# Kernel tuning notes

Measured on AMD Instinct MI355X. Metric: run time of the kernel, lower is better.

Reference implementation:

```python
import jax, jax.numpy as jnp
import numpy as np

DIM = 512
HEADS = 8
DIM_HEAD = 64
INNER = HEADS * DIM_HEAD  # 512
LN_EPS = 1e-5


def setup_inputs() -> dict:
    key = jax.random.key(0)
    ks = jax.random.split(key, 6)
    b, n = 2, 2048
    x = jax.random.normal(ks[0], (b, n, DIM), dtype=jnp.float32)
    # to_qkv: Linear(dim, inner*3, bias=False); torch weight is [out,in], apply as x @ W.T
    w_qkv = jax.random.normal(ks[1], (3 * INNER, DIM), dtype=jnp.float32) * (DIM ** -0.5)
    reattn_w = jax.random.normal(ks[2], (HEADS, HEADS), dtype=jnp.float32)
    ln_g = jnp.ones((HEADS,), dtype=jnp.float32)
    ln_b = jnp.zeros((HEADS,), dtype=jnp.float32)
    w_out = jax.random.normal(ks[3], (DIM, INNER), dtype=jnp.float32) * (INNER ** -0.5)
    b_out = jnp.zeros((DIM,), dtype=jnp.float32)
    return {"x": x, "w_qkv": w_qkv, "reattn_w": reattn_w,
            "ln_g": ln_g, "ln_b": ln_b, "w_out": w_out, "b_out": b_out}


def reference(x, w_qkv, reattn_w, ln_g, ln_b, w_out, b_out):
    b, n, _ = x.shape
    scale = DIM_HEAD ** -0.5
    qkv = x @ w_qkv.T  # [b, n, 3*inner]
    q, k, v = jnp.split(qkv, 3, axis=-1)
    # b n (h d) -> b h n d
    split_heads = lambda t: t.reshape(b, n, HEADS, DIM_HEAD).transpose(0, 2, 1, 3)
    q, k, v = split_heads(q), split_heads(k), split_heads(v)
    dots = jnp.einsum('bhid,bhjd->bhij', q, k) * scale
    attn = jax.nn.softmax(dots, axis=-1)
    # re-attention: cross-head mixing then LayerNorm over head dim
    attn = jnp.einsum('bhij,hg->bgij', attn, reattn_w)
    a = attn.transpose(0, 2, 3, 1)  # b i j h
    mu = jnp.mean(a, axis=-1, keepdims=True)
    var = jnp.mean((a - mu) ** 2, axis=-1, keepdims=True)
    a = (a - mu) * jax.lax.rsqrt(var + LN_EPS) * ln_g + ln_b
    attn = a.transpose(0, 3, 1, 2)  # b h i j
    out = jnp.einsum('bhij,bhjd->bhid', attn, v)
    out = out.transpose(0, 2, 1, 3).reshape(b, n, INNER)
    out = out @ w_out.T + b_out  # dropout p=0 -> identity
    return out
```

## Files before the change

kernel.cpp:

```cpp
#include <hip/hip_runtime.h>
#include <hip/hip_bf16.h>


typedef __attribute__((ext_vector_type(8))) short bfx8;
typedef __attribute__((ext_vector_type(4))) float f32x4;
typedef unsigned short u16;
typedef unsigned int u32;

#define QSCALE 0.18033688011112042f

static __device__ inline u16 f2bf(float f) {
  union { float f; unsigned u; } cv; cv.f = f;
  unsigned u = cv.u;
  u += 0x7fffu + ((u >> 16) & 1u);
  return (u16)(u >> 16);
}
static __device__ inline u32 cvtpk(float lo, float hi) {
  u32 d; asm("v_cvt_pk_bf16_f32 %0, %1, %2" : "=v"(d) : "v"(lo), "v"(hi)); return d;
}
static __device__ inline float fexp2(float x) {
  float r; asm("v_exp_f32 %0, %1" : "=v"(r) : "v"(x)); return r;
}
static __device__ inline float flog2(float x) {
  float r; asm("v_log_f32 %0, %1" : "=v"(r) : "v"(x)); return r;
}

__global__ __launch_bounds__(256) void convert3(
    const float* __restrict__ x, const float* __restrict__ wq,
    const float* __restrict__ wo,
    u16* __restrict__ xb, u16* __restrict__ wqb, u16* __restrict__ wob) {
  int e = (blockIdx.x * 256 + threadIdx.x) * 4;
  const float* src; u16* dst; int off;
  if (e < 2097152)      { src = x;  dst = xb;  off = e; }
  else if (e < 2883584) { src = wq; dst = wqb; off = e - 2097152; }
  else                  { src = wo; dst = wob; off = e - 2883584; }
  float4 v = *(const float4*)&src[off];
  ushort4 o; o.x = f2bf(v.x); o.y = f2bf(v.y); o.z = f2bf(v.z); o.w = f2bf(v.w);
  *(ushort4*)&dst[off] = o;
}

__global__ __launch_bounds__(256) void gemm_qkv(
    const u16* __restrict__ A, const u16* __restrict__ B,
    u16* __restrict__ qb, u16* __restrict__ kb, u16* __restrict__ vtb) {
  __shared__ u16 As[128 * 32];
  __shared__ u16 Bs[128 * 32];
  const int t = threadIdx.x, lane = t & 63;
  const int wm = (t >> 6) >> 1, wn = (t >> 6) & 1;
  const int m0 = blockIdx.y * 128, n0 = blockIdx.x * 128;
  const int li = lane & 15, lg = lane >> 4;
  const int rowA = t >> 2, kb8 = (t & 3) * 8;
  f32x4 acc[4][4] = {};
  for (int k0 = 0; k0 < 512; k0 += 32) {
    __syncthreads();
    *(bfx8*)&As[rowA * 32 + kb8]        = *(const bfx8*)&A[(size_t)(m0 + rowA) * 512 + k0 + kb8];
    *(bfx8*)&As[(rowA + 64) * 32 + kb8] = *(const bfx8*)&A[(size_t)(m0 + rowA + 64) * 512 + k0 + kb8];
    *(bfx8*)&Bs[rowA * 32 + kb8]        = *(const bfx8*)&B[(size_t)(n0 + rowA) * 512 + k0 + kb8];
    *(bfx8*)&Bs[(rowA + 64) * 32 + kb8] = *(const bfx8*)&B[(size_t)(n0 + rowA + 64) * 512 + k0 + kb8];
    __syncthreads();
    bfx8 af[4], bf_[4];
#pragma unroll
    for (int mi = 0; mi < 4; mi++)
      af[mi] = *(const bfx8*)&As[(wm * 64 + mi * 16 + li) * 32 + lg * 8];
#pragma unroll
    for (int ni = 0; ni < 4; ni++)
      bf_[ni] = *(const bfx8*)&Bs[(wn * 64 + ni * 16 + li) * 32 + lg * 8];
#pragma unroll
    for (int mi = 0; mi < 4; mi++)
#pragma unroll
      for (int ni = 0; ni < 4; ni++)
        acc[mi][ni] = __builtin_amdgcn_mfma_f32_16x16x32_bf16(af[mi], bf_[ni], acc[mi][ni], 0, 0, 0);
  }
#pragma unroll
  for (int mi = 0; mi < 4; mi++) {
#pragma unroll
    for (int ni = 0; ni < 4; ni++) {
      const int nc  = n0 + wn * 64 + ni * 16 + li;
      const int mrb = m0 + wm * 64 + mi * 16 + lg * 4;
      const int part = nc >> 9, within = nc & 511;
      const int h = within >> 6, d = within & 63;
      const int bb = mrb >> 11, ii = mrb & 2047;
      if (part == 0) {
#pragma unroll
        for (int r = 0; r < 4; r++)
          qb[(((size_t)bb * 8 + h) * 2048 + ii + r) * 64 + d] = f2bf(acc[mi][ni][r] * QSCALE);
      } else if (part == 1) {
#pragma unroll
        for (int r = 0; r < 4; r++)
          kb[(((size_t)bb * 8 + h) * 2048 + ii + r) * 64 + d] = f2bf(acc[mi][ni][r]);
      } else {
        ushort4 u;
        u.x = f2bf(acc[mi][ni][0]); u.y = f2bf(acc[mi][ni][1]);
        u.z = f2bf(acc[mi][ni][2]); u.w = f2bf(acc[mi][ni][3]);
        *(ushort4*)&vtb[(((size_t)bb * 8 + h) * 64 + d) * 2048 + ii] = u;
      }
    }
  }
}

__global__ __launch_bounds__(256) void passA(
    const u16* __restrict__ qb, const u16* __restrict__ kb,
    float2* __restrict__ statp) {
  const int t = threadIdx.x, lane = t & 63, w = t >> 6;
  const int bh = blockIdx.y, js = blockIdx.z;
  const int i0 = blockIdx.x * 64 + w * 16;
  const int li = lane & 15, lg = lane >> 4;
  const u16* Qh = qb + ((size_t)bh * 2048 + i0 + li) * 64;
  const u16* Kb = kb + (size_t)bh * 2048 * 64;
  const bfx8 q0 = *(const bfx8*)&Qh[lg * 8];
  const bfx8 q1 = *(const bfx8*)&Qh[32 + lg * 8];
  float m = -1e30f, l = 0.f;
  const int jbeg = js * 512, jend = jbeg + 512;
  for (int j0 = jbeg; j0 < jend; j0 += 32) {
    const u16* KhA = Kb + (size_t)(j0 + li) * 64;
    const u16* KhB = KhA + 16 * 64;
    bfx8 a0 = *(const bfx8*)&KhA[lg * 8];
    bfx8 a1 = *(const bfx8*)&KhA[32 + lg * 8];
    bfx8 b0 = *(const bfx8*)&KhB[lg * 8];
    bfx8 b1 = *(const bfx8*)&KhB[32 + lg * 8];
    __builtin_amdgcn_sched_barrier(0);
    f32x4 sa = {0.f, 0.f, 0.f, 0.f}, sb = {0.f, 0.f, 0.f, 0.f};
    sa = __builtin_amdgcn_mfma_f32_16x16x32_bf16(a0, q0, sa, 0, 0, 0);
    sa = __builtin_amdgcn_mfma_f32_16x16x32_bf16(a1, q1, sa, 0, 0, 0);
    sb = __builtin_amdgcn_mfma_f32_16x16x32_bf16(b0, q0, sb, 0, 0, 0);
    sb = __builtin_amdgcn_mfma_f32_16x16x32_bf16(b1, q1, sb, 0, 0, 0);
    float mt = fmaxf(fmaxf(fmaxf(sa[0], sa[1]), fmaxf(sa[2], sa[3])),
                     fmaxf(fmaxf(sb[0], sb[1]), fmaxf(sb[2], sb[3])));
    float mn = fmaxf(m, mt);
    float es = (fexp2(sa[0] - mn) + fexp2(sa[1] - mn)) + (fexp2(sa[2] - mn) + fexp2(sa[3] - mn))
             + (fexp2(sb[0] - mn) + fexp2(sb[1] - mn)) + (fexp2(sb[2] - mn) + fexp2(sb[3] - mn));
    l = fmaf(l, fexp2(m - mn), es);
    m = mn;
  }
  for (int off = 16; off < 64; off <<= 1) {
    float mo = __shfl_xor(m, off, 64);
    float lo = __shfl_xor(l, off, 64);
    float mn = fmaxf(m, mo);
    l = l * fexp2(m - mn) + lo * fexp2(mo - mn);
    m = mn;
  }
  if (lane < 16) statp[(size_t)js * 32768 + (size_t)bh * 2048 + i0 + li] = make_float2(m, l);
}

__global__ __launch_bounds__(512) void kFused(
    const u16* __restrict__ qb, const u16* __restrict__ kb,
    const u16* __restrict__ vtb, const float2* __restrict__ statp,
    const float* __restrict__ Wmix, const float* __restrict__ lng,
    const float* __restrict__ lnb, float* __restrict__ innerF) {
  __shared__ __align__(16) u16 Spk[64 * 512];
  __shared__ __align__(16) u16 A2h[8 * 64 * 72];
  __shared__ float stMs[64 * 8];
  const int t = threadIdx.x, lane = t & 63, w = t >> 6;
  const int li = lane & 15, lg = lane >> 4;
  const int ig = blockIdx.x * 64, b = blockIdx.y, j0 = blockIdx.z * 512;

  float wm_[8][8], lng_[8], lnb_[8];
#pragma unroll
  for (int h = 0; h < 8; h++)
#pragma unroll
    for (int g = 0; g < 8; g++) wm_[h][g] = Wmix[h * 8 + g];
#pragma unroll
  for (int g = 0; g < 8; g++) { lng_[g] = lng[g]; lnb_[g] = lnb[g]; }

  {
    const int i = t >> 3, h = t & 7;
    const size_t idx = ((size_t)(b * 8 + h)) * 2048 + ig + i;
    float m = -1e30f, l = 0.f;
#pragma unroll
    for (int z = 0; z < 4; z++) {
      const float2 a = statp[(size_t)z * 32768 + idx];
      const float mn = fmaxf(m, a.x);
      l = l * fexp2(m - mn) + a.y * fexp2(a.x - mn);
      m = mn;
    }
    stMs[i * 8 + h] = m + flog2(l);
  }

  bfx8 qf[4][2];
#pragma unroll
  for (int ii = 0; ii < 4; ii++)
#pragma unroll
    for (int ks = 0; ks < 2; ks++)
      qf[ii][ks] = *(const bfx8*)&qb[(((size_t)(b * 8 + w)) * 2048 + ig + ii * 16 + li) * 64
                                     + ks * 32 + lg * 8];
  __syncthreads();
  float stMp[4];
#pragma unroll
  for (int ii = 0; ii < 4; ii++) stMp[ii] = stMs[(ii * 16 + li) * 8 + w];

  f32x4 pacc[4][4] = {};
  const int mixI = t >> 3, mixJ8 = (t & 7) * 8;
  const int mixSwz = (mixI & 7) << 3;
  for (int jt = j0; jt < j0 + 512; jt += 64) {
    bfx8 vf0[4];
#pragma unroll
    for (int dt = 0; dt < 4; dt++)
      vf0[dt] = *(const bfx8*)&vtb[(((size_t)(b * 8 + w)) * 64 + dt * 16 + li) * 2048
                                   + jt + lg * 8];
    __builtin_amdgcn_sched_barrier(0);
    bfx8 kf[4][2];
#pragma unroll
    for (int ji = 0; ji < 4; ji++)
#pragma unroll
      for (int ks = 0; ks < 2; ks++)
        kf[ji][ks] = *(const bfx8*)&kb[(((size_t)(b * 8 + w)) * 2048 + jt + ji * 16 + li) * 64
                                       + ks * 32 + lg * 8];
    __builtin_amdgcn_sched_barrier(0);
#pragma unroll
    for (int ii = 0; ii < 4; ii++) {
      f32x4 s[4] = {};
#pragma unroll
      for (int ji = 0; ji < 4; ji++) {
        s[ji] = __builtin_amdgcn_mfma_f32_16x16x32_bf16(kf[ji][0], qf[ii][0], s[ji], 0, 0, 0);
        s[ji] = __builtin_amdgcn_mfma_f32_16x16x32_bf16(kf[ji][1], qf[ii][1], s[ji], 0, 0, 0);
      }
      const int i = ii * 16 + li;
      const int swzI = (i & 7) << 3;
#pragma unroll
      for (int ji = 0; ji < 4; ji++) {
        const float p0 = fexp2(s[ji][0] - stMp[ii]);
        const float p1 = fexp2(s[ji][1] - stMp[ii]);
        const float p2 = fexp2(s[ji][2] - stMp[ii]);
        const float p3 = fexp2(s[ji][3] - stMp[ii]);
        const int x = (ji * 16 + lg * 4) ^ swzI;
        *(uint2*)&Spk[i * 512 + w * 64 + x] = make_uint2(cvtpk(p0, p1), cvtpk(p2, p3));
      }
    }
    __syncthreads();
    {
      u32 ogw[8][4];
      float tmp[8];
#pragma unroll
      for (int hf = 0; hf < 2; hf++) {
        float p[8][4];
#pragma unroll
        for (int h = 0; h < 8; h++) {
          const int x4 = (mixJ8 + hf * 4) ^ mixSwz;
          const uint2 v = *(const uint2*)&Spk[mixI * 512 + h * 64 + x4];
          union { u32 u; float f; } c0, c1, c2, c3;
          c0.u = v.x << 16; c1.u = v.x & 0xffff0000u;
          c2.u = v.y << 16; c3.u = v.y & 0xffff0000u;
          p[h][0] = c0.f; p[h][1] = c1.f; p[h][2] = c2.f; p[h][3] = c3.f;
        }
#pragma unroll
        for (int e = 0; e < 4; e++) {
          float a_[8]; float sum = 0.f, sumsq = 0.f;
#pragma unroll
          for (int g = 0; g < 8; g++) {
            float acc = 0.f;
#pragma unroll
            for (int h = 0; h < 8; h++) acc = fmaf(p[h][e], wm_[h][g], acc);
            a_[g] = acc; sum += acc; sumsq = fmaf(acc, acc, sumsq);
          }
          const float mu = sum * 0.125f;
          const float var = fmaf(sumsq, 0.125f, -mu * mu);
          const float rs = rsqrtf(var + 1e-5f);
#pragma unroll
          for (int g = 0; g < 8; g++) {
            const float av = fmaf((a_[g] - mu) * rs, lng_[g], lnb_[g]);
            if (e & 1) ogw[g][hf * 2 + (e >> 1)] = cvtpk(tmp[g], av);
            else       tmp[g] = av;
          }
        }
      }
#pragma unroll
      for (int g = 0; g < 8; g++)
        *(uint4*)&A2h[g * 4608 + mixI * 72 + (mixJ8 ^ mixSwz)] =
            make_uint4(ogw[g][0], ogw[g][1], ogw[g][2], ogw[g][3]);
    }
    __syncthreads();
    bfx8 vf1[4];
#pragma unroll
    for (int dt = 0; dt < 4; dt++)
      vf1[dt] = *(const bfx8*)&vtb[(((size_t)(b * 8 + w)) * 64 + dt * 16 + li) * 2048
                                   + jt + 32 + lg * 8];
    __builtin_amdgcn_sched_barrier(0);
    __builtin_amdgcn_s_setprio(1);
#pragma unroll
    for (int iSub = 0; iSub < 4; iSub++) {
      const bfx8 af0 = *(const bfx8*)&A2h[w * 4608 + (iSub * 16 + li) * 72
                                          + ((lg * 8) ^ ((li & 7) << 3))];
#pragma unroll
      for (int dt = 0; dt < 4; dt++)
        pacc[iSub][dt] = __builtin_amdgcn_mfma_f32_16x16x32_bf16(af0, vf0[dt], pacc[iSub][dt], 0, 0, 0);
    }
#pragma unroll
    for (int iSub = 0; iSub < 4; iSub++) {
      const bfx8 af1 = *(const bfx8*)&A2h[w * 4608 + (iSub * 16 + li) * 72
                                          + ((32 + lg * 8) ^ ((li & 7) << 3))];
#pragma unroll
      for (int dt = 0; dt < 4; dt++)
        pacc[iSub][dt] = __builtin_amdgcn_mfma_f32_16x16x32_bf16(af1, vf1[dt], pacc[iSub][dt], 0, 0, 0);
    }
    __builtin_amdgcn_s_setprio(0);
    __syncthreads();
  }
#pragma unroll
  for (int iSub = 0; iSub < 4; iSub++)
#pragma unroll
    for (int dt = 0; dt < 4; dt++)
#pragma unroll
      for (int r = 0; r < 4; r++)
        atomicAdd(&innerF[((size_t)b * 2048 + ig + iSub * 16 + lg * 4 + r) * 512
                          + w * 64 + dt * 16 + li],
                  pacc[iSub][dt][r]);
}

__global__ __launch_bounds__(256) void convertInner(
    const float* __restrict__ inF, u16* __restrict__ outB) {
  int e = (blockIdx.x * 256 + threadIdx.x) * 4;
  float4 v = *(const float4*)&inF[e];
  ushort4 o; o.x = f2bf(v.x); o.y = f2bf(v.y); o.z = f2bf(v.z); o.w = f2bf(v.w);
  *(ushort4*)&outB[e] = o;
}

__global__ __launch_bounds__(256) void gemm_out(
    const u16* __restrict__ A, const u16* __restrict__ B,
    float* __restrict__ outf, const float* __restrict__ bias) {
  __shared__ u16 As[128 * 32];
  __shared__ u16 Bs[128 * 32];
  const int t = threadIdx.x, lane = t & 63;
  const int wm = (t >> 6) >> 1, wn = (t >> 6) & 1;
  const int m0 = blockIdx.y * 128, n0 = blockIdx.x * 128;
  const int li = lane & 15, lg = lane >> 4;
  const int rowA = t >> 2, kb8 = (t & 3) * 8;
  f32x4 acc[4][4] = {};
  for (int k0 = 0; k0 < 512; k0 += 32) {
    __syncthreads();
    *(bfx8*)&As[rowA * 32 + kb8]        = *(const bfx8*)&A[(size_t)(m0 + rowA) * 512 + k0 + kb8];
    *(bfx8*)&As[(rowA + 64) * 32 + kb8] = *(const bfx8*)&A[(size_t)(m0 + rowA + 64) * 512 + k0 + kb8];
    *(bfx8*)&Bs[rowA * 32 + kb8]        = *(const bfx8*)&B[(size_t)(n0 + rowA) * 512 + k0 + kb8];
    *(bfx8*)&Bs[(rowA + 64) * 32 + kb8] = *(const bfx8*)&B[(size_t)(n0 + rowA + 64) * 512 + k0 + kb8];
    __syncthreads();
    bfx8 af[4], bf_[4];
#pragma unroll
    for (int mi = 0; mi < 4; mi++)
      af[mi] = *(const bfx8*)&As[(wm * 64 + mi * 16 + li) * 32 + lg * 8];
#pragma unroll
    for (int ni = 0; ni < 4; ni++)
      bf_[ni] = *(const bfx8*)&Bs[(wn * 64 + ni * 16 + li) * 32 + lg * 8];
#pragma unroll
    for (int mi = 0; mi < 4; mi++)
#pragma unroll
      for (int ni = 0; ni < 4; ni++)
        acc[mi][ni] = __builtin_amdgcn_mfma_f32_16x16x32_bf16(af[mi], bf_[ni], acc[mi][ni], 0, 0, 0);
  }
#pragma unroll
  for (int mi = 0; mi < 4; mi++) {
#pragma unroll
    for (int ni = 0; ni < 4; ni++) {
      const int nc  = n0 + wn * 64 + ni * 16 + li;
      const int mrb = m0 + wm * 64 + mi * 16 + lg * 4;
      const float bv = bias[nc];
#pragma unroll
      for (int r = 0; r < 4; r++)
        outf[(size_t)(mrb + r) * 512 + nc] = acc[mi][ni][r] + bv;
    }
  }
}

extern "C" void kernel_launch(void* const* d_in, const int* in_sizes, int n_in,
                              void* d_out, int out_size, void* d_ws, size_t ws_size,
                              hipStream_t stream) {
  const float* x      = (const float*)d_in[0];
  const float* w_qkv  = (const float*)d_in[1];
  const float* reattn = (const float*)d_in[2];
  const float* ln_g   = (const float*)d_in[3];
  const float* ln_b   = (const float*)d_in[4];
  const float* w_out  = (const float*)d_in[5];
  const float* b_out  = (const float*)d_in[6];
  float* out = (float*)d_out;
  char* ws = (char*)d_ws;
  u16*    xb    = (u16*)(ws + 0);
  u16*    wqb   = (u16*)(ws + 4194304);
  float*  innerF= (float*)(ws + 0);
  u16*    qbf   = (u16*)(ws + 8388608);
  u16*    kbf   = (u16*)(ws + 12582912);
  u16*    vtb   = (u16*)(ws + 16777216);
  float2* statp = (float2*)(ws + 20971520);
  u16*    wob   = (u16*)(ws + 22020096);
  u16*    innerB= (u16*)(ws + 8388608);

  convert3<<<3072, 256, 0, stream>>>(x, w_qkv, w_out, xb, wqb, wob);
  gemm_qkv<<<dim3(12, 32), 256, 0, stream>>>(xb, wqb, qbf, kbf, vtb);
  hipMemsetAsync(innerF, 0, 8388608, stream);
  passA<<<dim3(32, 16, 4), 256, 0, stream>>>(qbf, kbf, statp);
  kFused<<<dim3(32, 2, 4), 512, 0, stream>>>(qbf, kbf, vtb, statp, reattn, ln_g, ln_b, innerF);
  convertInner<<<2048, 256, 0, stream>>>(innerF, innerB);
  gemm_out<<<dim3(4, 32), 256, 0, stream>>>(innerB, wob, out, b_out);
}
```

Before: 204.5 us.

## Fuse fp32-to-bf16 conversion into GEMM loads and prefetch K tiles in fused attention

The separate convert3 kernel is removed. Both GEMMs now read fp32 x and weights directly and pack them to bf16 with v_cvt_pk_bf16_f32 while staging into LDS, which saves a launch and a full write and read of the bf16 copies. In the fused attention kernel the K fragments for the next tile are issued before the mixing phase, and both V halves are loaded at the start of each iteration, so global latency is hidden behind LDS and LayerNorm work. The cost is more register pressure and twice the global bytes per GEMM tile load. Rounding also changes slightly, from manual round-to-nearest-even to the hardware pack.

```diff
diff --git a/kernel.cpp b/kernel.cpp
--- a/kernel.cpp
+++ b/kernel.cpp
@@ -24,23 +24,13 @@
 static __device__ inline float flog2(float x) {
   float r; asm("v_log_f32 %0, %1" : "=v"(r) : "v"(x)); return r;
 }
-
-__global__ __launch_bounds__(256) void convert3(
-    const float* __restrict__ x, const float* __restrict__ wq,
-    const float* __restrict__ wo,
-    u16* __restrict__ xb, u16* __restrict__ wqb, u16* __restrict__ wob) {
-  int e = (blockIdx.x * 256 + threadIdx.x) * 4;
-  const float* src; u16* dst; int off;
-  if (e < 2097152)      { src = x;  dst = xb;  off = e; }
-  else if (e < 2883584) { src = wq; dst = wqb; off = e - 2097152; }
-  else                  { src = wo; dst = wob; off = e - 2883584; }
-  float4 v = *(const float4*)&src[off];
-  ushort4 o; o.x = f2bf(v.x); o.y = f2bf(v.y); o.z = f2bf(v.z); o.w = f2bf(v.w);
-  *(ushort4*)&dst[off] = o;
+static __device__ inline uint4 pk8(const float* p) {
+  float4 a = *(const float4*)p, b = *(const float4*)(p + 4);
+  return make_uint4(cvtpk(a.x, a.y), cvtpk(a.z, a.w), cvtpk(b.x, b.y), cvtpk(b.z, b.w));
 }
 
 __global__ __launch_bounds__(256) void gemm_qkv(
-    const u16* __restrict__ A, const u16* __restrict__ B,
+    const float* __restrict__ A, const float* __restrict__ B,
     u16* __restrict__ qb, u16* __restrict__ kb, u16* __restrict__ vtb) {
   __shared__ u16 As[128 * 32];
   __shared__ u16 Bs[128 * 32];
@@ -52,10 +42,10 @@
   f32x4 acc[4][4] = {};
   for (int k0 = 0; k0 < 512; k0 += 32) {
     __syncthreads();
-    *(bfx8*)&As[rowA * 32 + kb8]        = *(const bfx8*)&A[(size_t)(m0 + rowA) * 512 + k0 + kb8];
-    *(bfx8*)&As[(rowA + 64) * 32 + kb8] = *(const bfx8*)&A[(size_t)(m0 + rowA + 64) * 512 + k0 + kb8];
-    *(bfx8*)&Bs[rowA * 32 + kb8]        = *(const bfx8*)&B[(size_t)(n0 + rowA) * 512 + k0 + kb8];
-    *(bfx8*)&Bs[(rowA + 64) * 32 + kb8] = *(const bfx8*)&B[(size_t)(n0 + rowA + 64) * 512 + k0 + kb8];
+    *(uint4*)&As[rowA * 32 + kb8]        = pk8(&A[(size_t)(m0 + rowA) * 512 + k0 + kb8]);
+    *(uint4*)&As[(rowA + 64) * 32 + kb8] = pk8(&A[(size_t)(m0 + rowA + 64) * 512 + k0 + kb8]);
+    *(uint4*)&Bs[rowA * 32 + kb8]        = pk8(&B[(size_t)(n0 + rowA) * 512 + k0 + kb8]);
+    *(uint4*)&Bs[(rowA + 64) * 32 + kb8] = pk8(&B[(size_t)(n0 + rowA + 64) * 512 + k0 + kb8]);
     __syncthreads();
     bfx8 af[4], bf_[4];
 #pragma unroll
@@ -190,20 +180,24 @@
   f32x4 pacc[4][4] = {};
   const int mixI = t >> 3, mixJ8 = (t & 7) * 8;
   const int mixSwz = (mixI & 7) << 3;
+
+  bfx8 kf[4][2];
+#pragma unroll
+  for (int ji = 0; ji < 4; ji++)
+#pragma unroll
+    for (int ks = 0; ks < 2; ks++)
+      kf[ji][ks] = *(const bfx8*)&kb[(((size_t)(b * 8 + w)) * 2048 + j0 + ji * 16 + li) * 64
+                                     + ks * 32 + lg * 8];
+
   for (int jt = j0; jt < j0 + 512; jt += 64) {
-    bfx8 vf0[4];
-#pragma unroll
-    for (int dt = 0; dt < 4; dt++)
+    bfx8 vf0[4], vf1[4];
+#pragma unroll
+    for (int dt = 0; dt < 4; dt++) {
       vf0[dt] = *(const bfx8*)&vtb[(((size_t)(b * 8 + w)) * 64 + dt * 16 + li) * 2048
                                    + jt + lg * 8];
-    __builtin_amdgcn_sched_barrier(0);
-    bfx8 kf[4][2];
-#pragma unroll
-    for (int ji = 0; ji < 4; ji++)
-#pragma unroll
-      for (int ks = 0; ks < 2; ks++)
-        kf[ji][ks] = *(const bfx8*)&kb[(((size_t)(b * 8 + w)) * 2048 + jt + ji * 16 + li) * 64
-                                       + ks * 32 + lg * 8];
+      vf1[dt] = *(const bfx8*)&vtb[(((size_t)(b * 8 + w)) * 64 + dt * 16 + li) * 2048
+                                   + jt + 32 + lg * 8];
+    }
     __builtin_amdgcn_sched_barrier(0);
 #pragma unroll
     for (int ii = 0; ii < 4; ii++) {
@@ -225,6 +219,16 @@
         *(uint2*)&Spk[i * 512 + w * 64 + x] = make_uint2(cvtpk(p0, p1), cvtpk(p2, p3));
       }
     }
+    {
+      const int jn = (jt + 64 < j0 + 512) ? jt + 64 : j0;
+#pragma unroll
+      for (int ji = 0; ji < 4; ji++)
+#pragma unroll
+        for (int ks = 0; ks < 2; ks++)
+          kf[ji][ks] = *(const bfx8*)&kb[(((size_t)(b * 8 + w)) * 2048 + jn + ji * 16 + li) * 64
+                                         + ks * 32 + lg * 8];
+      __builtin_amdgcn_sched_barrier(0);
+    }
     __syncthreads();
     {
       u32 ogw[8][4];
@@ -268,12 +272,6 @@
             make_uint4(ogw[g][0], ogw[g][1], ogw[g][2], ogw[g][3]);
     }
     __syncthreads();
-    bfx8 vf1[4];
-#pragma unroll
-    for (int dt = 0; dt < 4; dt++)
-      vf1[dt] = *(const bfx8*)&vtb[(((size_t)(b * 8 + w)) * 64 + dt * 16 + li) * 2048
-                                   + jt + 32 + lg * 8];
-    __builtin_amdgcn_sched_barrier(0);
     __builtin_amdgcn_s_setprio(1);
 #pragma unroll
     for (int iSub = 0; iSub < 4; iSub++) {
@@ -314,7 +312,7 @@
 }
 
 __global__ __launch_bounds__(256) void gemm_out(
-    const u16* __restrict__ A, const u16* __restrict__ B,
+    const u16* __restrict__ A, const float* __restrict__ B,
     float* __restrict__ outf, const float* __restrict__ bias) {
   __shared__ u16 As[128 * 32];
   __shared__ u16 Bs[128 * 32];
@@ -328,8 +326,8 @@
     __syncthreads();
     *(bfx8*)&As[rowA * 32 + kb8]        = *(const bfx8*)&A[(size_t)(m0 + rowA) * 512 + k0 + kb8];
     *(bfx8*)&As[(rowA + 64) * 32 + kb8] = *(const bfx8*)&A[(size_t)(m0 + rowA + 64) * 512 + k0 + kb8];
-    *(bfx8*)&Bs[rowA * 32 + kb8]        = *(const bfx8*)&B[(size_t)(n0 + rowA) * 512 + k0 + kb8];
-    *(bfx8*)&Bs[(rowA + 64) * 32 + kb8] = *(const bfx8*)&B[(size_t)(n0 + rowA + 64) * 512 + k0 + kb8];
+    *(uint4*)&Bs[rowA * 32 + kb8]        = pk8(&B[(size_t)(n0 + rowA) * 512 + k0 + kb8]);
+    *(uint4*)&Bs[(rowA + 64) * 32 + kb8] = pk8(&B[(size_t)(n0 + rowA + 64) * 512 + k0 + kb8]);
     __syncthreads();
     bfx8 af[4], bf_[4];
 #pragma unroll
@@ -370,21 +368,17 @@
   const float* b_out  = (const float*)d_in[6];
   float* out = (float*)d_out;
   char* ws = (char*)d_ws;
-  u16*    xb    = (u16*)(ws + 0);
-  u16*    wqb   = (u16*)(ws + 4194304);
   float*  innerF= (float*)(ws + 0);
   u16*    qbf   = (u16*)(ws + 8388608);
   u16*    kbf   = (u16*)(ws + 12582912);
   u16*    vtb   = (u16*)(ws + 16777216);
   float2* statp = (float2*)(ws + 20971520);
-  u16*    wob   = (u16*)(ws + 22020096);
   u16*    innerB= (u16*)(ws + 8388608);
 
-  convert3<<<3072, 256, 0, stream>>>(x, w_qkv, w_out, xb, wqb, wob);
-  gemm_qkv<<<dim3(12, 32), 256, 0, stream>>>(xb, wqb, qbf, kbf, vtb);
+  gemm_qkv<<<dim3(12, 32), 256, 0, stream>>>(x, w_qkv, qbf, kbf, vtb);
   hipMemsetAsync(innerF, 0, 8388608, stream);
   passA<<<dim3(32, 16, 4), 256, 0, stream>>>(qbf, kbf, statp);
   kFused<<<dim3(32, 2, 4), 512, 0, stream>>>(qbf, kbf, vtb, statp, reattn, ln_g, ln_b, innerF);
   convertInner<<<2048, 256, 0, stream>>>(innerF, innerB);
-  gemm_out<<<dim3(4, 32), 256, 0, stream>>>(innerB, wob, out, b_out);
-}
+  gemm_out<<<dim3(4, 32), 256, 0, stream>>>(innerB, w_out, out, b_out);
+}
```

After: 197.7 us. 3.3% less time.
